# Optimization experiments

Hardware: AMD Instinct MI355X
Metric: run time of the kernel (lower is better)

## Reference

```python
import jax, jax.numpy as jnp
import numpy as np

N = 50000
E = 800000
H = 4
C = 64
EPS = 1e-5

def _gat_layer(x, W, a_src, a_dst, bias, src, dst, n):
    # x: [N, F_in]; W: [F_in, H*C]
    h = (x @ W).reshape(n, H, C)                      # [N,H,C]
    asrc = jnp.einsum('nhc,hc->nh', h, a_src)         # [N,H]
    adst = jnp.einsum('nhc,hc->nh', h, a_dst)         # [N,H]
    e = jax.nn.leaky_relu(asrc[src] + adst[dst], 0.2) # [E,H]
    emax = jax.ops.segment_max(e, dst, num_segments=n)
    e = jnp.exp(e - emax[dst])
    denom = jax.ops.segment_sum(e, dst, num_segments=n)
    alpha = e / (denom[dst] + 1e-16)                  # [E,H]
    msg = h[src] * alpha[:, :, None]                  # [E,H,C]
    out = jax.ops.segment_sum(msg, dst, num_segments=n)
    return out.reshape(n, H * C) + bias

def _bn_eval(x, gamma, beta, mean, var):
    return (x - mean) * jax.lax.rsqrt(var + EPS) * gamma + beta

def setup_inputs() -> dict:
    key = jax.random.key(0)
    ks = jax.random.split(key, 12)
    d = {}
    d['x'] = jax.random.normal(ks[0], (N, 128), jnp.float32)
    d['edge_index'] = jax.random.randint(ks[1], (2, E), 0, N, jnp.int32)
    d['W1'] = jax.random.normal(ks[2], (128, H * C), jnp.float32) * 0.05
    d['a_src1'] = jax.random.normal(ks[3], (H, C), jnp.float32) * 0.05
    d['a_dst1'] = jax.random.normal(ks[4], (H, C), jnp.float32) * 0.05
    d['b1'] = jnp.zeros((H * C,), jnp.float32)
    d['g1'] = jax.random.uniform(ks[5], (H * C,), jnp.float32, 0.5, 1.5)
    d['be1'] = jnp.zeros((H * C,), jnp.float32)
    d['m1'] = jnp.zeros((H * C,), jnp.float32)
    d['v1'] = jax.random.uniform(ks[6], (H * C,), jnp.float32, 0.5, 1.5)
    d['W2'] = jax.random.normal(ks[7], (H * C, H * C), jnp.float32) * 0.05
    d['a_src2'] = jax.random.normal(ks[8], (H, C), jnp.float32) * 0.05
    d['a_dst2'] = jax.random.normal(ks[9], (H, C), jnp.float32) * 0.05
    d['b2'] = jnp.zeros((H * C,), jnp.float32)
    d['g2'] = jax.random.uniform(ks[10], (H * C,), jnp.float32, 0.5, 1.5)
    d['be2'] = jnp.zeros((H * C,), jnp.float32)
    d['m2'] = jnp.zeros((H * C,), jnp.float32)
    d['v2'] = jax.random.uniform(ks[11], (H * C,), jnp.float32, 0.5, 1.5)
    return d

def reference(x, edge_index, W1, a_src1, a_dst1, b1, g1, be1, m1, v1,
              W2, a_src2, a_dst2, b2, g2, be2, m2, v2):
    # PyG GATConv default: add self-loops
    loops = jnp.arange(N, dtype=edge_index.dtype)
    src = jnp.concatenate([edge_index[0], loops])
    dst = jnp.concatenate([edge_index[1], loops])
    h = _gat_layer(x, W1, a_src1, a_dst1, b1, src, dst, N)
    h = jax.nn.relu(_bn_eval(h, g1, be1, m1, v1))  # dropout identity at eval
    h = _gat_layer(h, W2, a_src2, a_dst2, b2, src, dst, N)
    h = jax.nn.relu(_bn_eval(h, g2, be2, m2, v2))
    return jax.nn.log_softmax(h, axis=1)
```

## Files before the change

### kernel.cpp

```cpp
#include <hip/hip_runtime.h>
#include <hip/hip_bf16.h>
#include <cstdint>

#define N_NODES 50000
#define N_EDGES 800000
#define ET_EDGES (N_EDGES + N_NODES)
#define FDIM 256
#define BN_EPS 1e-5f
#define CAP 96

typedef short bf16x8 __attribute__((ext_vector_type(8)));
typedef float f32x4 __attribute__((ext_vector_type(4)));

__device__ __forceinline__ float lrelu(float x) { return x >= 0.f ? x : 0.2f * x; }
__device__ __forceinline__ float b2f(unsigned short u) {
    return __uint_as_float(((unsigned int)u) << 16);
}
__device__ __forceinline__ unsigned short f2b(float f) {
    unsigned int u = __float_as_uint(f);
    u += 0x7fffu + ((u >> 16) & 1u);
    return (unsigned short)(u >> 16);
}

__device__ __forceinline__ void acc_u8(float acc8[8], int2 p, float c) {
    unsigned px = (unsigned)p.x, py = (unsigned)p.y;
#pragma unroll
    for (int k = 0; k < 4; ++k)
        acc8[k] = fmaf((float)((unsigned char)(px >> (8 * k))), c, acc8[k]);
#pragma unroll
    for (int k = 0; k < 4; ++k)
        acc8[k + 4] = fmaf((float)((unsigned char)(py >> (8 * k))), c, acc8[k + 4]);
}

#define NB_CONV 6250
#define NB_WT1  128
#define NB_WT2  256
#define NB_DEGZ 196
__global__ __launch_bounds__(256) void setup_kernel(
        const float* __restrict__ x, unsigned short* __restrict__ xb,
        const float* __restrict__ W1, unsigned short* __restrict__ W1T,
        const float* __restrict__ W2, unsigned short* __restrict__ W2T,
        int* __restrict__ cursor,
        const float* __restrict__ b1, const float* __restrict__ g1,
        const float* __restrict__ be1, const float* __restrict__ m1,
        const float* __restrict__ v1,
        const float* __restrict__ b2, const float* __restrict__ g2,
        const float* __restrict__ be2, const float* __restrict__ m2,
        const float* __restrict__ v2,
        float* sc1, float* sh1, float* sc2, float* sh2) {
    int b = blockIdx.x, tid = threadIdx.x;
    if (b < NB_CONV) {
        int i = b * 256 + tid;
        float4 v = ((const float4*)x)[i];
        ushort4 o;
        o.x = f2b(v.x); o.y = f2b(v.y); o.z = f2b(v.z); o.w = f2b(v.w);
        ((ushort4*)xb)[i] = o;
    } else if (b < NB_CONV + NB_WT1) {
        int t = (b - NB_CONV) * 256 + tid;
        int n = t >> 7, k = t & 127;
        W1T[t] = f2b(W1[(size_t)k * 256 + n]);
    } else if (b < NB_CONV + NB_WT1 + NB_WT2) {
        int t = (b - NB_CONV - NB_WT1) * 256 + tid;
        int n = t >> 8, k = t & 255;
        W2T[t] = f2b(W2[(size_t)k * 256 + n]);
    } else if (b < NB_CONV + NB_WT1 + NB_WT2 + NB_DEGZ) {
        int i = (b - NB_CONV - NB_WT1 - NB_WT2) * 256 + tid;
        if (i < N_NODES) cursor[i] = 0;
    } else {
        int f = tid;
        float s1 = rsqrtf(v1[f] + BN_EPS) * g1[f];
        sc1[f] = s1;
        sh1[f] = (b1[f] - m1[f]) * s1 + be1[f];
        float s2 = rsqrtf(v2[f] + BN_EPS) * g2[f];
        sc2[f] = s2;
        sh2[f] = (b2[f] - m2[f]) * s2 + be2[f];
    }
}

__global__ __launch_bounds__(256) void scatter_kernel(const int* __restrict__ ei,
                                                      int* __restrict__ cursor,
                                                      int* __restrict__ csr) {
    int e = blockIdx.x * 256 + threadIdx.x;
    if (e >= ET_EDGES) return;
    int s, d;
    if (e < N_EDGES) { s = ei[e]; d = ei[N_EDGES + e]; }
    else             { s = d = e - N_EDGES; }
    int pos = atomicAdd(&cursor[d], 1);
    if (pos < CAP) csr[d * CAP + pos] = s;
}

template <int K>
__global__ __launch_bounds__(512) void gemm_fused_kernel(
        const unsigned short* __restrict__ A,
        const unsigned short* __restrict__ BT,
        const float* __restrict__ a_src, const float* __restrict__ a_dst,
        signed char* __restrict__ H8, float* __restrict__ scaleRow,
        float* __restrict__ asrc, float* __restrict__ adst, int M) {
    constexpr int BK = 64;
    __shared__ unsigned short As[128][BK + 8];
    __shared__ unsigned short Bs[256][BK + 8];
    __shared__ int amaxL[128];
    const int tid = threadIdx.x;
    const int lane = tid & 63;
    const int w = tid >> 6;
    const int bm = blockIdx.x * 128;
    const int wr = (w >> 2) * 64;
    const int wc = (w & 3) * 64;
    const int hd = w & 3;
    if (tid < 128) amaxL[tid] = 0;

    f32x4 acc[4][4];
#pragma unroll
    for (int i = 0; i < 4; ++i)
#pragma unroll
        for (int j = 0; j < 4; ++j) acc[i][j] = (f32x4){0.f, 0.f, 0.f, 0.f};

    const int srow = tid >> 3;
    const int skc = (tid & 7) * 8;

    for (int k0 = 0; k0 < K; k0 += BK) {
#pragma unroll
        for (int i = 0; i < 2; ++i) {
            int row = i * 64 + srow;
            int ar = bm + row; if (ar >= M) ar = M - 1;
            *(bf16x8*)&As[row][skc] = *(const bf16x8*)(A + (size_t)ar * K + k0 + skc);
        }
#pragma unroll
        for (int i = 0; i < 4; ++i) {
            int row = i * 64 + srow;
            *(bf16x8*)&Bs[row][skc] = *(const bf16x8*)(BT + (size_t)row * K + k0 + skc);
        }
        __syncthreads();
#pragma unroll
        for (int ks = 0; ks < BK; ks += 32) {
            const int kk = ks + (lane >> 4) * 8;
            bf16x8 af[4], bfr[4];
#pragma unroll
            for (int i = 0; i < 4; ++i) {
                af[i]  = *(const bf16x8*)&As[wr + i * 16 + (lane & 15)][kk];
                bfr[i] = *(const bf16x8*)&Bs[wc + i * 16 + (lane & 15)][kk];
            }
#pragma unroll
            for (int i = 0; i < 4; ++i)
#pragma unroll
                for (int j = 0; j < 4; ++j)
                    acc[i][j] = __builtin_amdgcn_mfma_f32_16x16x32_bf16(af[i], bfr[j], acc[i][j], 0, 0, 0);
        }
        __syncthreads();
    }

    const int q = lane >> 4, c16 = lane & 15;
#pragma unroll
    for (int i = 0; i < 4; ++i) {
#pragma unroll
        for (int r = 0; r < 4; ++r) {
            float a = fmaxf(fmaxf(fabsf(acc[i][0][r]), fabsf(acc[i][1][r])),
                            fmaxf(fabsf(acc[i][2][r]), fabsf(acc[i][3][r])));
#pragma unroll
            for (int off = 1; off < 16; off <<= 1) a = fmaxf(a, __shfl_xor(a, off));
            if (c16 == 0) atomicMax(&amaxL[wr + i * 16 + q * 4 + r], __float_as_int(a));
        }
    }
    __syncthreads();

    float asv[4], adv[4];
#pragma unroll
    for (int j = 0; j < 4; ++j) {
        int c = j * 16 + c16;
        asv[j] = a_src[hd * 64 + c];
        adv[j] = a_dst[hd * 64 + c];
    }
#pragma unroll
    for (int i = 0; i < 4; ++i) {
#pragma unroll
        for (int r = 0; r < 4; ++r) {
            int lrow = wr + i * 16 + q * 4 + r;
            int gr = bm + lrow;
            float amax = __int_as_float(amaxL[lrow]);
            float rcpS = amax > 1e-20f ? 127.f / amax : 0.f;
            if (gr < M) {
#pragma unroll
                for (int j = 0; j < 4; ++j) {
                    int qv = (int)rintf(acc[i][j][r] * rcpS);
                    H8[(size_t)gr * 256 + wc + j * 16 + c16] =
                        (signed char)(unsigned char)(qv + 128);
                }
                if (c16 == 0 && (w & 3) == 0) scaleRow[gr] = amax * (1.f / 127.f);
            }
            float p_s = acc[i][0][r] * asv[0] + acc[i][1][r] * asv[1]
                      + acc[i][2][r] * asv[2] + acc[i][3][r] * asv[3];
            float p_d = acc[i][0][r] * adv[0] + acc[i][1][r] * adv[1]
                      + acc[i][2][r] * adv[2] + acc[i][3][r] * adv[3];
#pragma unroll
            for (int off = 1; off < 16; off <<= 1) {
                p_s += __shfl_xor(p_s, off);
                p_d += __shfl_xor(p_d, off);
            }
            if (c16 == 0 && gr < M) {
                asrc[(size_t)gr * 4 + hd] = p_s;
                adst[(size_t)gr * 4 + hd] = p_d;
            }
        }
    }
}

template <bool FINAL>
__device__ __forceinline__ void gat_epilogue(const float acc8[8], int fl, bool doStore,
                                             int node, const float* __restrict__ scale,
                                             const float* __restrict__ shift,
                                             float* __restrict__ outf,
                                             unsigned short* __restrict__ outb) {
    float4 scA = ((const float4*)scale)[fl * 2], scB = ((const float4*)scale)[fl * 2 + 1];
    float4 shA = ((const float4*)shift)[fl * 2], shB = ((const float4*)shift)[fl * 2 + 1];
    float t[8];
    t[0] = fmaxf(fmaf(acc8[0], scA.x, shA.x), 0.f);
    t[1] = fmaxf(fmaf(acc8[1], scA.y, shA.y), 0.f);
    t[2] = fmaxf(fmaf(acc8[2], scA.z, shA.z), 0.f);
    t[3] = fmaxf(fmaf(acc8[3], scA.w, shA.w), 0.f);
    t[4] = fmaxf(fmaf(acc8[4], scB.x, shB.x), 0.f);
    t[5] = fmaxf(fmaf(acc8[5], scB.y, shB.y), 0.f);
    t[6] = fmaxf(fmaf(acc8[6], scB.z, shB.z), 0.f);
    t[7] = fmaxf(fmaf(acc8[7], scB.w, shB.w), 0.f);
    if (FINAL) {
        float m = t[0];
#pragma unroll
        for (int k = 1; k < 8; ++k) m = fmaxf(m, t[k]);
#pragma unroll
        for (int off = 1; off < 32; off <<= 1) m = fmaxf(m, __shfl_xor(m, off));
        float es = 0.f;
#pragma unroll
        for (int k = 0; k < 8; ++k) es += __expf(t[k] - m);
#pragma unroll
        for (int off = 1; off < 32; off <<= 1) es += __shfl_xor(es, off);
        float lse = m + logf(es);
        if (doStore) {
            float* p = outf + (size_t)node * 256 + fl * 8;
            *(float4*)p = make_float4(t[0] - lse, t[1] - lse, t[2] - lse, t[3] - lse);
            *(float4*)(p + 4) = make_float4(t[4] - lse, t[5] - lse, t[6] - lse, t[7] - lse);
        }
    } else {
        if (doStore) {
            bf16x8 ob;
#pragma unroll
            for (int k = 0; k < 8; ++k) ob[k] = (short)f2b(t[k]);
            *(bf16x8*)(outb + (size_t)node * 256 + fl * 8) = ob;
        }
    }
}

template <bool FINAL>
__global__ __launch_bounds__(256) void gat_gather_kernel(
        const int* __restrict__ cursor,
        const int* __restrict__ csr,
        const float* __restrict__ asrc,
        const float* __restrict__ adst,
        const float* __restrict__ scaleRow,
        const signed char* __restrict__ h8,
        const float* __restrict__ scale,
        const float* __restrict__ shift,
        float* __restrict__ outf,
        unsigned short* __restrict__ outb) {
    __shared__ int2 sa[4][4][65];

    const int wid = threadIdx.x >> 6;
    const int lane = threadIdx.x & 63;
    const int g = lane >> 5, l32 = lane & 31;
    const int hsel = l32 >> 3;
    const unsigned fo = (unsigned)(l32 << 3);

    const int nodeBase = blockIdx.x * 8 + wid * 2;
    if (nodeBase >= N_NODES) return;

    {
        int node = nodeBase + g;
        bool valid = node < N_NODES;
        int nodeC = valid ? node : N_NODES - 1;
        int deg = valid ? min(cursor[nodeC], CAP) : 0;
        int beg = nodeC * CAP;
        int dmax = max(deg, __shfl_xor(deg, 32));

        if (dmax <= 32) {
            float4 ad = *(const float4*)(adst + (size_t)nodeC * 4);
            int s = 0;
            float sc = 0.f;
            float c0 = -3.4e38f, c1 = -3.4e38f, c2 = -3.4e38f, c3 = -3.4e38f;
            if (l32 < deg) {
                s = csr[beg + l32];
                sc = scaleRow[s];
                float4 as = *(const float4*)(asrc + (size_t)s * 4);
                c0 = lrelu(as.x + ad.x); c1 = lrelu(as.y + ad.y);
                c2 = lrelu(as.z + ad.z); c3 = lrelu(as.w + ad.w);
            }
            float m0 = c0, m1 = c1, m2 = c2, m3 = c3;
#pragma unroll
            for (int off = 1; off < 32; off <<= 1) {
                m0 = fmaxf(m0, __shfl_xor(m0, off)); m1 = fmaxf(m1, __shfl_xor(m1, off));
                m2 = fmaxf(m2, __shfl_xor(m2, off)); m3 = fmaxf(m3, __shfl_xor(m3, off));
            }
            float e0 = 0.f, e1 = 0.f, e2 = 0.f, e3 = 0.f;
            if (l32 < deg) {
                e0 = __expf(c0 - m0); e1 = __expf(c1 - m1);
                e2 = __expf(c2 - m2); e3 = __expf(c3 - m3);
            }
            float s0 = e0, s1 = e1, s2 = e2, s3 = e3;
#pragma unroll
            for (int off = 1; off < 32; off <<= 1) {
                s0 += __shfl_xor(s0, off); s1 += __shfl_xor(s1, off);
                s2 += __shfl_xor(s2, off); s3 += __shfl_xor(s3, off);
            }
            float a0 = e0 / (s0 + 1e-16f) * sc, a1 = e1 / (s1 + 1e-16f) * sc;
            float a2 = e2 / (s2 + 1e-16f) * sc, a3 = e3 / (s3 + 1e-16f) * sc;
            sa[wid][0][lane] = make_int2(s, __float_as_int(a0));
            sa[wid][1][lane] = make_int2(s, __float_as_int(a1));
            sa[wid][2][lane] = make_int2(s, __float_as_int(a2));
            sa[wid][3][lane] = make_int2(s, __float_as_int(a3));
            float t0 = a0, t1 = a1, t2 = a2, t3 = a3;
#pragma unroll
            for (int off = 1; off < 32; off <<= 1) {
                t0 += __shfl_xor(t0, off); t1 += __shfl_xor(t1, off);
                t2 += __shfl_xor(t2, off); t3 += __shfl_xor(t3, off);
            }
            float corr = 128.f * (hsel == 0 ? t0 : hsel == 1 ? t1 : hsel == 2 ? t2 : t3);
            __asm__ volatile("s_waitcnt lgkmcnt(0)" ::: "memory");

            const int2* sal = &sa[wid][hsel][g * 32];
            float acc8[8];
#pragma unroll
            for (int k = 0; k < 8; ++k) acc8[k] = 0.f;

            int e = 0;
            for (; e + 7 < deg; e += 8) {
                int2 sv[8]; int2 hv[8];
#pragma unroll
                for (int u = 0; u < 8; ++u) sv[u] = sal[e + u];
#pragma unroll
                for (int u = 0; u < 8; ++u)
                    hv[u] = *(const int2*)(h8 + (((unsigned)sv[u].x << 8) + fo));
#pragma unroll
                for (int u = 0; u < 8; ++u) acc_u8(acc8, hv[u], __int_as_float(sv[u].y));
            }
            for (; e + 3 < deg; e += 4) {
                int2 sv[4]; int2 hv[4];
#pragma unroll
                for (int u = 0; u < 4; ++u) sv[u] = sal[e + u];
#pragma unroll
                for (int u = 0; u < 4; ++u)
                    hv[u] = *(const int2*)(h8 + (((unsigned)sv[u].x << 8) + fo));
#pragma unroll
                for (int u = 0; u < 4; ++u) acc_u8(acc8, hv[u], __int_as_float(sv[u].y));
            }
            for (; e < deg; ++e) {
                int2 sv = sal[e];
                int2 hA = *(const int2*)(h8 + (((unsigned)sv.x << 8) + fo));
                acc_u8(acc8, hA, __int_as_float(sv.y));
            }
#pragma unroll
            for (int k = 0; k < 8; ++k) acc8[k] -= corr;
            gat_epilogue<FINAL>(acc8, l32, valid, node, scale, shift, outf, outb);
            return;
        }
    }

    for (int t = 0; t < 2; ++t) {
        int fnode = nodeBase + t;
        if (fnode >= N_NODES) break;
        int fdeg = min(cursor[fnode], CAP);
        int fbeg = fnode * CAP, fend = fbeg + fdeg;
        float4 ad = *(const float4*)(adst + (size_t)fnode * 4);
        float acc8[8];
#pragma unroll
        for (int k = 0; k < 8; ++k) acc8[k] = 0.f;
        float corr;

        if (fdeg <= 64) {
            int s = 0;
            float sc = 0.f;
            float c0 = -3.4e38f, c1 = -3.4e38f, c2 = -3.4e38f, c3 = -3.4e38f;
            if (lane < fdeg) {
                s = csr[fbeg + lane];
                sc = scaleRow[s];
                float4 as = *(const float4*)(asrc + (size_t)s * 4);
                c0 = lrelu(as.x + ad.x); c1 = lrelu(as.y + ad.y);
                c2 = lrelu(as.z + ad.z); c3 = lrelu(as.w + ad.w);
            }
            float m0 = c0, m1 = c1, m2 = c2, m3 = c3;
#pragma unroll
            for (int off = 1; off < 64; off <<= 1) {
                m0 = fmaxf(m0, __shfl_xor(m0, off)); m1 = fmaxf(m1, __shfl_xor(m1, off));
                m2 = fmaxf(m2, __shfl_xor(m2, off)); m3 = fmaxf(m3, __shfl_xor(m3, off));
            }
            float e0 = 0.f, e1 = 0.f, e2 = 0.f, e3 = 0.f;
            if (lane < fdeg) {
                e0 = __expf(c0 - m0); e1 = __expf(c1 - m1);
                e2 = __expf(c2 - m2); e3 = __expf(c3 - m3);
            }
            float s0 = e0, s1 = e1, s2 = e2, s3 = e3;
#pragma unroll
            for (int off = 1; off < 64; off <<= 1) {
                s0 += __shfl_xor(s0, off); s1 += __shfl_xor(s1, off);
                s2 += __shfl_xor(s2, off); s3 += __shfl_xor(s3, off);
            }
            float a0 = e0 / (s0 + 1e-16f) * sc, a1 = e1 / (s1 + 1e-16f) * sc;
            float a2 = e2 / (s2 + 1e-16f) * sc, a3 = e3 / (s3 + 1e-16f) * sc;
            sa[wid][0][lane] = make_int2(s, __float_as_int(a0));
            sa[wid][1][lane] = make_int2(s, __float_as_int(a1));
            sa[wid][2][lane] = make_int2(s, __float_as_int(a2));
            sa[wid][3][lane] = make_int2(s, __float_as_int(a3));
            float t0 = a0, t1 = a1, t2 = a2, t3 = a3;
#pragma unroll
            for (int off = 1; off < 64; off <<= 1) {
                t0 += __shfl_xor(t0, off); t1 += __shfl_xor(t1, off);
                t2 += __shfl_xor(t2, off); t3 += __shfl_xor(t3, off);
            }
            corr = 128.f * (hsel == 0 ? t0 : hsel == 1 ? t1 : hsel == 2 ? t2 : t3);
            __asm__ volatile("s_waitcnt lgkmcnt(0)" ::: "memory");

            const int2* sal = &sa[wid][hsel][0];
            int e = 0;
            for (; e + 1 < fdeg; e += 2) {
                int2 sv = sal[e + g];
                int2 hA = *(const int2*)(h8 + (((unsigned)sv.x << 8) + fo));
                acc_u8(acc8, hA, __int_as_float(sv.y));
            }
            if (e < fdeg) {
                int idx = e + g;
                int2 sv = sal[idx < fdeg ? idx : 0];
                float aA = idx < fdeg ? __int_as_float(sv.y) : 0.f;
                int2 hA = *(const int2*)(h8 + (((unsigned)sv.x << 8) + fo));
                acc_u8(acc8, hA, aA);
            }
#pragma unroll
            for (int k = 0; k < 8; ++k) acc8[k] += __shfl_xor(acc8[k], 32);
        } else {
            float m0 = -3.4e38f, m1 = -3.4e38f, m2 = -3.4e38f, m3 = -3.4e38f;
            for (int e = fbeg + lane; e < fend; e += 64) {
                int s = csr[e];
                float4 as = *(const float4*)(asrc + (size_t)s * 4);
                m0 = fmaxf(m0, lrelu(as.x + ad.x)); m1 = fmaxf(m1, lrelu(as.y + ad.y));
                m2 = fmaxf(m2, lrelu(as.z + ad.z)); m3 = fmaxf(m3, lrelu(as.w + ad.w));
            }
#pragma unroll
            for (int off = 1; off < 64; off <<= 1) {
                m0 = fmaxf(m0, __shfl_xor(m0, off)); m1 = fmaxf(m1, __shfl_xor(m1, off));
                m2 = fmaxf(m2, __shfl_xor(m2, off)); m3 = fmaxf(m3, __shfl_xor(m3, off));
            }
            float s0 = 0.f, s1 = 0.f, s2 = 0.f, s3 = 0.f;
            for (int e = fbeg + lane; e < fend; e += 64) {
                int s = csr[e];
                float4 as = *(const float4*)(asrc + (size_t)s * 4);
                s0 += __expf(lrelu(as.x + ad.x) - m0); s1 += __expf(lrelu(as.y + ad.y) - m1);
                s2 += __expf(lrelu(as.z + ad.z) - m2); s3 += __expf(lrelu(as.w + ad.w) - m3);
            }
#pragma unroll
            for (int off = 1; off < 64; off <<= 1) {
                s0 += __shfl_xor(s0, off); s1 += __shfl_xor(s1, off);
                s2 += __shfl_xor(s2, off); s3 += __shfl_xor(s3, off);
            }
            float mh = (hsel == 0) ? m0 : (hsel == 1) ? m1 : (hsel == 2) ? m2 : m3;
            float rh = (hsel == 0) ? 1.f / (s0 + 1e-16f) : (hsel == 1) ? 1.f / (s1 + 1e-16f)
                     : (hsel == 2) ? 1.f / (s2 + 1e-16f) : 1.f / (s3 + 1e-16f);
            float adh = (hsel == 0) ? ad.x : (hsel == 1) ? ad.y : (hsel == 2) ? ad.z : ad.w;
            float asumL = 0.f;
            for (int e = fbeg; e < fend; ++e) {
                int s = csr[e];
                float ash = asrc[(size_t)s * 4 + hsel];
                float a = __expf(lrelu(ash + adh) - mh) * rh * scaleRow[s];
                asumL += a;
                int2 hv = *(const int2*)(h8 + (((unsigned)s << 8) + fo));
                acc_u8(acc8, hv, a);
            }
            corr = 128.f * asumL;
        }
#pragma unroll
        for (int k = 0; k < 8; ++k) acc8[k] -= corr;
        gat_epilogue<FINAL>(acc8, l32, g == 0, fnode, scale, shift, outf, outb);
    }
}

extern "C" void kernel_launch(void* const* d_in, const int* in_sizes, int n_in,
                              void* d_out, int out_size, void* d_ws, size_t ws_size,
                              hipStream_t stream) {
    (void)in_sizes; (void)n_in; (void)out_size; (void)ws_size;
    const float* x   = (const float*)d_in[0];
    const int*   ei  = (const int*)d_in[1];
    const float* W1  = (const float*)d_in[2];
    const float* as1 = (const float*)d_in[3];
    const float* ad1 = (const float*)d_in[4];
    const float* b1  = (const float*)d_in[5];
    const float* g1  = (const float*)d_in[6];
    const float* be1 = (const float*)d_in[7];
    const float* m1  = (const float*)d_in[8];
    const float* v1  = (const float*)d_in[9];
    const float* W2  = (const float*)d_in[10];
    const float* as2 = (const float*)d_in[11];
    const float* ad2 = (const float*)d_in[12];
    const float* b2  = (const float*)d_in[13];
    const float* g2  = (const float*)d_in[14];
    const float* be2 = (const float*)d_in[15];
    const float* m2  = (const float*)d_in[16];
    const float* v2  = (const float*)d_in[17];

    float* out = (float*)d_out;
    unsigned short* actb = (unsigned short*)d_out;

    char* base = (char*)d_ws;
    signed char* h8 = (signed char*)base;          base += (size_t)N_NODES * 256;
    float* scaleRow = (float*)base;                base += (size_t)N_NODES * 4;
    unsigned short* xb  = (unsigned short*)base;   base += (size_t)N_NODES * 128 * 2;
    float* asrc = (float*)base;                    base += (size_t)N_NODES * 4 * 4;
    float* adst = (float*)base;                    base += (size_t)N_NODES * 4 * 4;
    float* sc1 = (float*)base;                     base += 1024;
    float* sh1 = (float*)base;                     base += 1024;
    float* sc2 = (float*)base;                     base += 1024;
    float* sh2 = (float*)base;                     base += 1024;
    unsigned short* W1T = (unsigned short*)base;   base += 256 * 128 * 2;
    unsigned short* W2T = (unsigned short*)base;   base += 256 * 256 * 2;
    int* cursor = (int*)base;                      base += N_NODES * 4;
    int* csr  = (int*)base;

    setup_kernel<<<NB_CONV + NB_WT1 + NB_WT2 + NB_DEGZ + 1, 256, 0, stream>>>(
        x, xb, W1, W1T, W2, W2T, cursor,
        b1, g1, be1, m1, v1, b2, g2, be2, m2, v2, sc1, sh1, sc2, sh2);

    const int eb = (ET_EDGES + 255) / 256;
    scatter_kernel<<<eb, 256, 0, stream>>>(ei, cursor, csr);

    const int gb = (N_NODES + 127) / 128;
    const int nb = (N_NODES + 7) / 8;

    gemm_fused_kernel<128><<<gb, 512, 0, stream>>>(xb, W1T, as1, ad1, h8, scaleRow,
                                                   asrc, adst, N_NODES);
    gat_gather_kernel<false><<<nb, 256, 0, stream>>>(cursor, csr, asrc, adst, scaleRow, h8,
                                                     sc1, sh1, nullptr, actb);

    gemm_fused_kernel<256><<<gb, 512, 0, stream>>>(actb, W2T, as2, ad2, h8, scaleRow,
                                                   asrc, adst, N_NODES);
    gat_gather_kernel<true><<<nb, 256, 0, stream>>>(cursor, csr, asrc, adst, scaleRow, h8,
                                                    sc2, sh2, out, nullptr);
}
```

Before: 318.6 us.

## Merge edge scatter into first GEMM launch as extra blocks

Removes the separate CSR scatter kernel and appends extra blocks to the first fused GEMM launch that perform the edge-to-bucket atomic scatter, four edges per thread. The intent is to overlap the latency-bound atomic scatter with the compute-bound GEMM and save one kernel launch. The scatter blocks share the GEMM's 512-thread launch bounds and its static shared memory allocation, which may limit occupancy for those blocks.

```diff
diff --git a/kernel.cpp b/kernel.cpp
--- a/kernel.cpp
+++ b/kernel.cpp
@@ -77,30 +77,42 @@
     }
 }
 
-__global__ __launch_bounds__(256) void scatter_kernel(const int* __restrict__ ei,
-                                                      int* __restrict__ cursor,
-                                                      int* __restrict__ csr) {
-    int e = blockIdx.x * 256 + threadIdx.x;
-    if (e >= ET_EDGES) return;
-    int s, d;
-    if (e < N_EDGES) { s = ei[e]; d = ei[N_EDGES + e]; }
-    else             { s = d = e - N_EDGES; }
-    int pos = atomicAdd(&cursor[d], 1);
-    if (pos < CAP) csr[d * CAP + pos] = s;
-}
-
 template <int K>
 __global__ __launch_bounds__(512) void gemm_fused_kernel(
         const unsigned short* __restrict__ A,
         const unsigned short* __restrict__ BT,
         const float* __restrict__ a_src, const float* __restrict__ a_dst,
         signed char* __restrict__ H8, float* __restrict__ scaleRow,
-        float* __restrict__ asrc, float* __restrict__ adst, int M) {
+        float* __restrict__ asrc, float* __restrict__ adst, int M,
+        const int* __restrict__ ei, int* __restrict__ cursor,
+        int* __restrict__ csr, int gemmBlocks) {
     constexpr int BK = 64;
     __shared__ unsigned short As[128][BK + 8];
     __shared__ unsigned short Bs[256][BK + 8];
     __shared__ int amaxL[128];
     const int tid = threadIdx.x;
+
+    if (blockIdx.x >= gemmBlocks) {
+        const int base = (blockIdx.x - gemmBlocks) * 2048 + tid;
+        int sv[4], dv[4], pv[4];
+        bool ok[4];
+#pragma unroll
+        for (int u = 0; u < 4; ++u) {
+            int e = base + u * 512;
+            ok[u] = e < ET_EDGES;
+            int ec = ok[u] ? e : 0;
+            if (ec < N_EDGES) { sv[u] = ei[ec]; dv[u] = ei[N_EDGES + ec]; }
+            else              { sv[u] = dv[u] = ec - N_EDGES; }
+        }
+#pragma unroll
+        for (int u = 0; u < 4; ++u)
+            if (ok[u]) pv[u] = atomicAdd(&cursor[dv[u]], 1);
+#pragma unroll
+        for (int u = 0; u < 4; ++u)
+            if (ok[u] && pv[u] < CAP) csr[dv[u] * CAP + pv[u]] = sv[u];
+        return;
+    }
+
     const int lane = tid & 63;
     const int w = tid >> 6;
     const int bm = blockIdx.x * 128;
@@ -522,19 +534,19 @@
         x, xb, W1, W1T, W2, W2T, cursor,
         b1, g1, be1, m1, v1, b2, g2, be2, m2, v2, sc1, sh1, sc2, sh2);
 
-    const int eb = (ET_EDGES + 255) / 256;
-    scatter_kernel<<<eb, 256, 0, stream>>>(ei, cursor, csr);
-
     const int gb = (N_NODES + 127) / 128;
+    const int nsb = (ET_EDGES + 2047) / 2048;
     const int nb = (N_NODES + 7) / 8;
 
-    gemm_fused_kernel<128><<<gb, 512, 0, stream>>>(xb, W1T, as1, ad1, h8, scaleRow,
-                                                   asrc, adst, N_NODES);
+    gemm_fused_kernel<128><<<gb + nsb, 512, 0, stream>>>(xb, W1T, as1, ad1, h8, scaleRow,
+                                                         asrc, adst, N_NODES,
+                                                         ei, cursor, csr, gb);
     gat_gather_kernel<false><<<nb, 256, 0, stream>>>(cursor, csr, asrc, adst, scaleRow, h8,
                                                      sc1, sh1, nullptr, actb);
 
     gemm_fused_kernel<256><<<gb, 512, 0, stream>>>(actb, W2T, as2, ad2, h8, scaleRow,
-                                                   asrc, adst, N_NODES);
+                                                   asrc, adst, N_NODES,
+                                                   ei, cursor, csr, gb);
     gat_gather_kernel<true><<<nb, 256, 0, stream>>>(cursor, csr, asrc, adst, scaleRow, h8,
                                                     sc2, sh2, out, nullptr);
 }
```

New measurement: 324.1 us. About the same (+1.7%).
